# Kernel tuning notes

Measured on AMD Instinct MI355X. Metric: run time of the kernel, lower is better.

The kernel has to match this reference:

```python
import jax, jax.numpy as jnp
import numpy as np

T, B, H = 1024, 128, 256


def setup_inputs() -> dict:
    key = jax.random.key(0)
    k1, k2, k3, k4, k5 = jax.random.split(key, 5)
    ins = jax.random.normal(k1, (T, B, H), dtype=jnp.float32)
    resets = jax.random.randint(k2, (T, B), 0, 2).astype(jnp.bool_)
    # GRUCell params (flax layout): input dense (with bias) and recurrent dense
    # (bias only on the candidate 'hn' branch). Orthogonal-ish init approximated
    # by scaled normal for a pure-jnp reference.
    s = 1.0 / np.sqrt(H)
    Wi = jax.random.normal(k3, (H, 3 * H), dtype=jnp.float32) * s   # -> [ir|iz|in]
    Wh = jax.random.normal(k4, (H, 3 * H), dtype=jnp.float32) * s   # -> [hr|hz|hn]
    bi = jnp.zeros((3 * H,), dtype=jnp.float32)
    bhn = jnp.zeros((H,), dtype=jnp.float32)
    h0 = jnp.zeros((B, H), dtype=jnp.float32)  # initialize_carry -> zeros
    return {"ins": ins, "resets": resets, "h0": h0,
            "Wi": Wi, "Wh": Wh, "bi": bi, "bhn": bhn}


def reference(ins, resets, h0, Wi, Wh, bi, bhn):
    """ScannedRNN: GRU recurrence over time with per-step reset masking.

    ins: [T,B,H], resets: [T,B] bool, h0: [B,H]. Returns (final_carry, ys).
    """
    Hh = h0.shape[-1]

    def step(h, xt):
        x_t, r_t = xt                              # [B,H], [B]
        h = jnp.where(r_t[:, None], 0.0, h)        # reset carry to zeros
        gi = x_t @ Wi + bi                         # [B,3H]
        gh = h @ Wh                                # [B,3H]
        i_r, i_z, i_n = gi[:, :Hh], gi[:, Hh:2 * Hh], gi[:, 2 * Hh:]
        h_r, h_z, h_n = gh[:, :Hh], gh[:, Hh:2 * Hh], gh[:, 2 * Hh:]
        r = jax.nn.sigmoid(i_r + h_r)
        z = jax.nn.sigmoid(i_z + h_z)
        n = jnp.tanh(i_n + r * (h_n + bhn))
        h_new = (1.0 - z) * n + z * h
        return h_new, h_new                        # GRUCell returns (carry, y=carry)

    h_final, ys = jax.lax.scan(step, h0, (ins, resets))
    return h_final, ys
```

## Files before the change

### kernel.cpp

```cpp
#include <hip/hip_runtime.h>


typedef _Float16 half2_t __attribute__((ext_vector_type(2)));
typedef _Float16 half4_t __attribute__((ext_vector_type(4)));
typedef _Float16 half8_t __attribute__((ext_vector_type(8)));
typedef float f32x4 __attribute__((ext_vector_type(4)));

#define T_DIM 1024
#define B_DIM 128
#define H_DIM 256
#define N3 768
#define NSTREAM 4096
#define ROWS 16

__device__ __forceinline__ int perm_n(int cp) {
  int ublk = cp / 48;
  int rem = cp % 48;
  int g = rem >> 4;
  int u4 = rem & 15;
  return g * 256 + ublk * 16 + u4;
}


__global__ void prep_whb(const float* __restrict__ Wh, unsigned* __restrict__ WhB) {
  int i = blockIdx.x * 256 + threadIdx.x;
  int h = 2 * i;
  int idx = h & 7;
  int lane = (h >> 3) & 63;
  int ntk = h >> 9;
  int nt = ntk % 48;
  int kt = ntk / 48;
  int k = kt * 32 + ((lane >> 4) * 8) + idx;
  int n = perm_n(nt * 16 + (lane & 15));
  half2_t p;
  p.x = (_Float16)Wh[(size_t)k * N3 + n];
  p.y = (_Float16)Wh[(size_t)(k + 1) * N3 + n];
  WhB[i] = __builtin_bit_cast(unsigned, p);
}

__global__ void prep_witp(const float* __restrict__ Wi, _Float16* __restrict__ WiTp) {
  int i = blockIdx.x * 256 + threadIdx.x;
  int cp = i >> 8;
  int k = i & 255;
  WiTp[(size_t)cp * 256 + k] = (_Float16)Wi[(size_t)k * N3 + perm_n(cp)];
}

__global__ void prep_bip(const float* __restrict__ bi, float* __restrict__ bip) {
  int i = threadIdx.x;
  bip[i] = bi[perm_n(i)];
}

__global__ void init_h(const float* __restrict__ h0, float* __restrict__ h_state) {
  int i = blockIdx.x * 256 + threadIdx.x;
  h_state[i] = h0[i];
}

__global__ __launch_bounds__(256) void conv_a(
    const float* __restrict__ src, _Float16* __restrict__ dst, int n8) {
  int i = blockIdx.x * 256 + threadIdx.x;
  const int stride = gridDim.x * 256;
  for (; i < n8; i += stride) {
    float4 a = ((const float4*)src)[2 * i];
    float4 b = ((const float4*)src)[2 * i + 1];
    half8_t h;
    h[0] = (_Float16)a.x; h[1] = (_Float16)a.y;
    h[2] = (_Float16)a.z; h[3] = (_Float16)a.w;
    h[4] = (_Float16)b.x; h[5] = (_Float16)b.y;
    h[6] = (_Float16)b.z; h[7] = (_Float16)b.w;
    ((half8_t*)dst)[i] = h;
  }
}


__global__ void seg_transpose(const int* __restrict__ resets, int* __restrict__ resT) {
  int i = blockIdx.x * 256 + threadIdx.x;
  int b = i >> 10;
  int t = i & 1023;
  resT[i] = resets[(size_t)t * B_DIM + b];
}

__global__ __launch_bounds__(256) void seg_extract(
    const int* __restrict__ resT, int t0, int steps,
    unsigned* __restrict__ rowsegs, unsigned* __restrict__ rowcnt,
    unsigned* __restrict__ lhist) {
  const int b = blockIdx.x;
  const int tid = threadIdx.x;
  const int lane = tid & 63;
  const int w = tid >> 6;
  const int per = (steps + 255) >> 8;

  __shared__ unsigned short sstartL[1025];
  __shared__ unsigned lcur[1025];
  __shared__ unsigned wsum[4];

  for (int l = tid; l <= steps; l += 256) lcur[l] = 0;

  const int* rrow = resT + (size_t)b * T_DIM + t0;
  int myfirst = tid * per;
  unsigned cnt = 0;
  for (int i = 0; i < per; ++i) {
    int s = myfirst + i;
    if (s < steps && (s == 0 || rrow[s] != 0)) cnt++;
  }
  unsigned pre = cnt;
#pragma unroll
  for (int off = 1; off < 64; off <<= 1) {
    unsigned v = __shfl_up(pre, off);
    if (lane >= off) pre += v;
  }
  if (lane == 63) wsum[w] = pre;
  __syncthreads();
  unsigned wbase = 0, total = 0;
#pragma unroll
  for (int i = 0; i < 4; ++i) {
    if (i < w) wbase += wsum[i];
    total += wsum[i];
  }
  unsigned r = wbase + pre - cnt;
  for (int i = 0; i < per; ++i) {
    int s = myfirst + i;
    if (s < steps && (s == 0 || rrow[s] != 0)) sstartL[r++] = (unsigned short)s;
  }
  if (tid == 0) { sstartL[total] = (unsigned short)steps; rowcnt[b] = total; }
  __syncthreads();

  const unsigned carry0 = (rrow[0] == 0) ? 1u : 0u;
  for (unsigned rr = tid; rr < total; rr += 256) {
    int st = sstartL[rr];
    int len = (int)sstartL[rr + 1] - st;
    unsigned carry = (st == 0) ? carry0 : 0u;
    unsigned rk = atomicAdd(&lcur[len], 1u);
    rowsegs[(size_t)b * T_DIM + rr] =
        (unsigned)st | ((unsigned)len << 10) | (rk << 21) | (carry << 31);
  }
  __syncthreads();
  for (int l = tid; l <= steps; l += 256) lhist[(size_t)l * 128 + b] = lcur[l];
}

__global__ __launch_bounds__(1024) void seg_prefix2(
    const unsigned* __restrict__ lhist, unsigned* __restrict__ rowoff,
    unsigned* __restrict__ cursors, unsigned* __restrict__ Warr,
    unsigned* __restrict__ nseg, int steps) {
  __shared__ unsigned cs[1024];
  __shared__ unsigned cs2[1024];
  const int tid = threadIdx.x;
  const int len = tid + 1;
  unsigned run = 0;
  if (len <= steps) {
    for (int b = 0; b < 128; ++b) {
      rowoff[(size_t)len * 128 + b] = run;
      run += lhist[(size_t)len * 128 + b];
    }
  }
  unsigned own = run;
  unsigned own2 = run * (unsigned)len;
  cs[tid] = own;
  cs2[tid] = own2;
  for (int off = 1; off < 1024; off <<= 1) {
    __syncthreads();
    unsigned v = (tid + off < 1024) ? cs[tid + off] : 0u;
    unsigned v2 = (tid + off < 1024) ? cs2[tid + off] : 0u;
    __syncthreads();
    cs[tid] += v;
    cs2[tid] += v2;
  }
  cursors[len] = cs[tid] - own;
  Warr[len] = cs2[tid] - own2;
  if (tid == 0) *nseg = cs[0];
}

__global__ void seg_scatter2(
    const unsigned* __restrict__ rowsegs, const unsigned* __restrict__ rowcnt,
    const unsigned* __restrict__ rowoff, const unsigned* __restrict__ cursors,
    unsigned* __restrict__ segs) {
  int i = blockIdx.x * 256 + threadIdx.x;
  int b = i >> 10;
  int rr = i & 1023;
  if ((unsigned)rr >= rowcnt[b]) return;
  unsigned rec = rowsegs[i];
  unsigned st = rec & 0x3FF;
  unsigned len = (rec >> 10) & 0x7FF;
  unsigned rk = (rec >> 21) & 0x3FF;
  unsigned carry = rec >> 31;
  unsigned dst = cursors[len] + rowoff[(size_t)len * 128 + b] + rk;
  segs[dst] = st | (len << 10) | ((unsigned)b << 21) | (carry << 28);
}

__global__ void str_mark(
    const unsigned* __restrict__ segs, const unsigned* __restrict__ nseg_p,
    const unsigned* __restrict__ cursors, const unsigned* __restrict__ Warr,
    unsigned* __restrict__ sstart, unsigned* __restrict__ preexS, int Q) {
  unsigned r = blockIdx.x * 256 + threadIdx.x;
  unsigned n = *nseg_p;
  if (r >= n) return;
  unsigned rec = segs[r];
  unsigned len = (rec >> 10) & 0x7FF;
  unsigned pre = Warr[len] + len * (r - cursors[len]);
  unsigned st = pre / (unsigned)Q;
  unsigned stp;
  if (r == 0) {
    sstart[0] = 0; preexS[0] = 0; stp = 0;
  } else {
    unsigned rec2 = segs[r - 1];
    unsigned len2 = (rec2 >> 10) & 0x7FF;
    unsigned pre2 = Warr[len2] + len2 * (r - 1 - cursors[len2]);
    stp = pre2 / (unsigned)Q;
  }
  for (unsigned s = stp + 1; s <= st; ++s) { sstart[s] = r; preexS[s] = pre; }
}

__global__ __launch_bounds__(256) void gi_gemm(
    const _Float16* __restrict__ A16,
    const _Float16* __restrict__ BT,
    const float* __restrict__ bip,
    _Float16* __restrict__ Cout,
    int M) {
  __shared__ _Float16 Al[128 * 32];
  __shared__ _Float16 Bl[128 * 32];
  const int tid = threadIdx.x;
  const int lane = tid & 63;
  const int w = tid >> 6;
  const int wr = w >> 1, wc = w & 1;
  const int m0 = blockIdx.y * 128;
  const int n0 = blockIdx.x * 128;

  const int srow = lane >> 2;
  const int schunk = lane & 3;

  f32x4 acc[4][4] = {};

  for (int ks = 0; ks < 256; ks += 32) {
#pragma unroll
    for (int rr = 0; rr < 2; ++rr) {
      const int row = w * 32 + rr * 16;
      __builtin_amdgcn_global_load_lds(
          (const __attribute__((address_space(1))) void*)
              ((const char*)A16 + ((size_t)(m0 + row + srow) * 256 + ks) * 2 + schunk * 16),
          (__attribute__((address_space(3))) void*)((char*)Al + row * 64),
          16, 0, 0);
      __builtin_amdgcn_global_load_lds(
          (const __attribute__((address_space(1))) void*)
              ((const char*)BT + ((size_t)(n0 + row + srow) * 256 + ks) * 2 + schunk * 16),
          (__attribute__((address_space(3))) void*)((char*)Bl + row * 64),
          16, 0, 0);
    }
    __syncthreads();

    half8_t af[4], bf[4];
#pragma unroll
    for (int m = 0; m < 4; ++m)
      af[m] = *(const half8_t*)&Al[(size_t)(wr * 64 + m * 16 + (lane & 15)) * 32 + (lane >> 4) * 8];
#pragma unroll
    for (int n = 0; n < 4; ++n)
      bf[n] = *(const half8_t*)&Bl[(size_t)(wc * 64 + n * 16 + (lane & 15)) * 32 + (lane >> 4) * 8];
#pragma unroll
    for (int m = 0; m < 4; ++m)
#pragma unroll
      for (int n = 0; n < 4; ++n)
        acc[m][n] = __builtin_amdgcn_mfma_f32_16x16x32_f16(af[m], bf[n], acc[m][n], 0, 0, 0);
    __syncthreads();
  }

#pragma unroll
  for (int m = 0; m < 4; ++m) {
    int row = m0 + wr * 64 + m * 16 + (lane >> 4) * 4;
#pragma unroll
    for (int n = 0; n < 4; ++n) {
      int col = n0 + wc * 64 + n * 16 + (lane & 15);
      float bv = bip[col];
#pragma unroll
      for (int r2 = 0; r2 < 4; ++r2)
        Cout[(size_t)(row + r2) * N3 + col] = (_Float16)(acc[m][n][r2] + bv);
    }
  }
}

__global__ __launch_bounds__(512)
__attribute__((amdgpu_waves_per_eu(1, 2)))
void scan_stream(
    const _Float16* __restrict__ WhB,
    const _Float16* __restrict__ gi,
    const unsigned* __restrict__ segs,
    const unsigned* __restrict__ sstart,
    const unsigned* __restrict__ preexS,
    const unsigned* __restrict__ nseg_ptr,
    const float* __restrict__ bhn,
    const float* __restrict__ h_in,
    float* __restrict__ h_out,
    float* __restrict__ ys,
    float* __restrict__ hfin,
    int t0, int steps, int Q) {
  __shared__ _Float16 h_lds[ROWS][264];
  __shared__ _Float16 giL[ROWS][776];
  __shared__ unsigned rst[ROWS];
  __shared__ unsigned rowrank[ROWS];
  __shared__ unsigned rowpw[ROWS];
  __shared__ unsigned rfresh[ROWS];
  __shared__ unsigned wava[8];

  const int tid = threadIdx.x;
  const int lane = tid & 63;
  const int w = tid >> 6;
  const int sbase = blockIdx.x * ROWS;
  const unsigned nseg = *nseg_ptr;

  if (tid < ROWS) {
    const unsigned st = sbase + tid;
    unsigned r = sstart[st], pw = preexS[st];
    unsigned v = 0u, rk = 0xFFFFFFFFu, rpw = 0u;
    if (r < nseg && pw < (st + 1) * (unsigned)Q) {
      unsigned rec = segs[r];
      unsigned len = (rec >> 10) & 0x7FF;
      v = (rec & 0x3FF) | (((rec >> 21) & 0x7F) << 10) | (len << 17) |
          (((rec >> 28) & 1u) << 28);
      rk = r; rpw = pw + len;
    }
    rst[tid] = v; rowrank[tid] = rk; rowpw[tid] = rpw; rfresh[tid] = 0;
  }
  if (tid < 8) wava[tid] = 1u;

  half8_t whr[48];
#pragma unroll
  for (int kt = 0; kt < 8; ++kt)
#pragma unroll
    for (int q = 0; q < 6; ++q)
      whr[kt * 6 + q] =
          *(const half8_t*)&WhB[(((size_t)kt * 48 + w * 6 + q) * 64 + lane) * 8];

  __syncthreads();
#pragma unroll
  for (int rr = 0; rr < 2; ++rr) {
    int row = 2 * w + rr;
    unsigned s = rst[row];
    float4 o = make_float4(0.f, 0.f, 0.f, 0.f);
    if (s & (1u << 28))
      o = *(const float4*)&h_in[(size_t)((s >> 10) & 0x7F) * 256 + lane * 4];
    half4_t hv;
    hv.x = (_Float16)o.x; hv.y = (_Float16)o.y;
    hv.z = (_Float16)o.z; hv.w = (_Float16)o.w;
    *(half4_t*)&h_lds[row][lane * 4] = hv;
  }

  const int r16 = lane & 15;
  const int q4 = (lane >> 4) * 4;
  const int kq8 = (lane >> 4) * 8;
  const int u0 = w * 32 + r16;
  const float bh0 = bhn[u0];
  const float bh1 = bhn[u0 + 16];

  while (true) {
    __syncthreads();
    unsigned alive = 0;
#pragma unroll
    for (int i = 0; i < 8; ++i) alive += wava[i];
    if (!alive) break;

#pragma unroll
    for (int rr = 0; rr < 2; ++rr) {
      const int row = 2 * w + rr;
      const unsigned ss = rst[row];
      if ((ss >> 17) & 0x7FF) {
        const char* src = (const char*)(gi +
            ((size_t)(ss & 0x3FF) * B_DIM + ((ss >> 10) & 0x7F)) * N3);
        char* dst = (char*)&giL[row][0];
#if __has_builtin(__builtin_amdgcn_global_load_lds)
        __builtin_amdgcn_global_load_lds(
            (const __attribute__((address_space(1))) void*)(src + (size_t)lane * 16),
            (__attribute__((address_space(3))) void*)dst, 16, 0, 0);
        __builtin_amdgcn_global_load_lds(
            (const __attribute__((address_space(1))) void*)(src + 1024 + (size_t)lane * 4),
            (__attribute__((address_space(3))) void*)(dst + 1024), 4, 0, 0);
        __builtin_amdgcn_global_load_lds(
            (const __attribute__((address_space(1))) void*)(src + 1280 + (size_t)lane * 4),
            (__attribute__((address_space(3))) void*)(dst + 1280), 4, 0, 0);
#else
        {
          uint4 a = *(const uint4*)(src + ((size_t)(lane & 31)) * 48);
          uint4 b = *(const uint4*)(src + ((size_t)(lane & 31)) * 48 + 16);
          uint4 c = *(const uint4*)(src + ((size_t)(lane & 31)) * 48 + 32);
          if ((lane >> 5) == 0) {
            char* d2 = dst + ((size_t)(lane & 31)) * 48;
            *(uint4*)(d2) = a; *(uint4*)(d2 + 16) = b; *(uint4*)(d2 + 32) = c;
          }
        }
#endif
      }
    }

    f32x4 acc[6] = {};
#pragma unroll
    for (int kt = 0; kt < 8; ++kt) {
      half8_t afr = *(const half8_t*)&h_lds[r16][kt * 32 + kq8];
#pragma unroll
      for (int q = 0; q < 6; ++q)
        acc[q] = __builtin_amdgcn_mfma_f32_16x16x32_f16(afr, whr[kt * 6 + q], acc[q], 0, 0, 0);
    }
    __syncthreads();

#pragma unroll
    for (int j = 0; j < 2; ++j) {
      const int u = u0 + j * 16;
      const int cb = w * 96 + j * 48 + r16;
      const float bh = j ? bh1 : bh0;
#pragma unroll
      for (int e = 0; e < 4; ++e) {
        const int row = q4 + e;
        if ((rst[row] >> 17) & 0x7FF) {
          const float gr = (float)giL[row][cb];
          const float gz = (float)giL[row][cb + 16];
          const float gn = (float)giL[row][cb + 32];
          const float sigr = 1.f / (1.f + __expf(-(gr + acc[3 * j][e])));
          const float sigz = 1.f / (1.f + __expf(-(gz + acc[3 * j + 1][e])));
          const float narg = gn + sigr * (acc[3 * j + 2][e] + bh);
          const float eo = __expf(-2.f * narg);
          const float nn = 2.f / (1.f + eo) - 1.f;
          const float hold = (float)h_lds[row][u];
          const float hnew = (1.f - sigz) * nn + sigz * hold;
          h_lds[row][u] = (_Float16)hnew;
        }
      }
    }
    __syncthreads();

    unsigned alv = 0;
#pragma unroll
    for (int rr = 0; rr < 2; ++rr) {
      const int row = 2 * w + rr;
      const unsigned sp = rst[row];
      const unsigned rem = (sp >> 17) & 0x7FF;
      if (rem) {
        const int t = sp & 0x3FF;
        const int b = (sp >> 10) & 0x7F;
        half4_t hv = *(const half4_t*)&h_lds[row][lane * 4];
        float4 o;
        o.x = (float)hv.x; o.y = (float)hv.y; o.z = (float)hv.z; o.w = (float)hv.w;
        *(float4*)&ys[(((size_t)(t0 + t) * B_DIM + b) * H_DIM) + lane * 4] = o;
        if (rem == 1) {
          if (t == steps - 1) *(float4*)&h_out[(size_t)b * 256 + lane * 4] = o;
          if (t0 + t == T_DIM - 1) *(float4*)&hfin[(size_t)b * 256 + lane * 4] = o;
        }
        if (lane == 0) {
          rfresh[row] = 0u;
          if (rem > 1) {
            rst[row] = (unsigned)(t + 1) | ((unsigned)b << 10) | ((rem - 1) << 17);
            alv++;
          } else {
            unsigned ns = 0u;
            const unsigned st = sbase + row;
            unsigned rn = rowrank[row] + 1, pw = rowpw[row];
            if (rn < nseg && pw < (st + 1) * (unsigned)Q) {
              unsigned rec = segs[rn];
              unsigned len = (rec >> 10) & 0x7FF;
              ns = (rec & 0x3FF) | (((rec >> 21) & 0x7F) << 10) | (len << 17) |
                   (((rec >> 28) & 1u) << 28);
              rowrank[row] = rn; rowpw[row] = pw + len;
              rfresh[row] = 1u;
              alv++;
            }
            rst[row] = ns;
          }
        }
      }
    }
    if (lane == 0) wava[w] = alv;
#pragma unroll
    for (int rr = 0; rr < 2; ++rr) {
      const int row = 2 * w + rr;
      if (rfresh[row]) {
        unsigned s = rst[row];
        float4 o = make_float4(0.f, 0.f, 0.f, 0.f);
        if (s & (1u << 28))
          o = *(const float4*)&h_in[(size_t)((s >> 10) & 0x7F) * 256 + lane * 4];
        half4_t hv;
        hv.x = (_Float16)o.x; hv.y = (_Float16)o.y;
        hv.z = (_Float16)o.z; hv.w = (_Float16)o.w;
        *(half4_t*)&h_lds[row][lane * 4] = hv;
      }
    }
  }
}

extern "C" void kernel_launch(void* const* d_in, const int* in_sizes, int n_in,
                              void* d_out, int out_size, void* d_ws, size_t ws_size,
                              hipStream_t stream) {
  const float* ins    = (const float*)d_in[0];
  const int*   resets = (const int*)d_in[1];
  const float* h0     = (const float*)d_in[2];
  const float* Wi     = (const float*)d_in[3];
  const float* Wh     = (const float*)d_in[4];
  const float* bi     = (const float*)d_in[5];
  const float* bhn    = (const float*)d_in[6];
  float* out  = (float*)d_out;
  float* hfin = out;
  float* ys   = out + B_DIM * H_DIM;

  char* ws = (char*)d_ws;
  unsigned*  WhB     = (unsigned*)(ws + 0);
  _Float16*  WiTp    = (_Float16*)(ws + 393216);
  float*     bip     = (float*)(ws + 786432);
  float*     hA      = (float*)(ws + 789504);
  float*     hB      = (float*)(ws + 920576);
  int*       resT    = (int*)(ws + 1051648);
  unsigned*  rowsegs = (unsigned*)(ws + 1575936);
  unsigned*  rowcnt  = (unsigned*)(ws + 2100224);
  unsigned*  lhist   = (unsigned*)(ws + 2100736);
  unsigned*  rowoff  = (unsigned*)(ws + 2625536);
  unsigned*  cursors = (unsigned*)(ws + 3150336);
  unsigned*  Warr    = (unsigned*)(ws + 3154560);
  unsigned*  nseg    = (unsigned*)(ws + 3158784);
  unsigned*  segs    = (unsigned*)(ws + 3158912);
  unsigned*  sstart  = (unsigned*)(ws + 3683200);
  unsigned*  preexS  = (unsigned*)(ws + 3748736);
  const size_t gi_off = 3814400;

  int CH = T_DIM;
  while (CH > 256) {
    size_t need = gi_off + (size_t)CH * 128 * (N3 + H_DIM) * 2;
    if (need <= ws_size) break;
    CH >>= 1;
  }
  _Float16* gibuf = (_Float16*)(ws + gi_off);
  _Float16* A16   = (_Float16*)(ws + gi_off + (size_t)CH * 128 * N3 * 2);

  prep_whb<<<384, 256, 0, stream>>>(Wh, WhB);
  prep_witp<<<768, 256, 0, stream>>>(Wi, WiTp);
  prep_bip<<<1, 768, 0, stream>>>(bi, bip);
  init_h<<<128, 256, 0, stream>>>(h0, hA);
  seg_transpose<<<512, 256, 0, stream>>>(resets, resT);

  float* hbufs[2] = {hA, hB};
  for (int c = 0, t0 = 0; t0 < T_DIM; ++c, t0 += CH) {
    int steps = (t0 + CH <= T_DIM) ? CH : (T_DIM - t0);
    int M = steps * B_DIM;
    int Q = (M + NSTREAM - 1) / NSTREAM;
    if (Q < 1) Q = 1;

    conv_a<<<2048, 256, 0, stream>>>(ins + (size_t)t0 * B_DIM * H_DIM, A16, M * 32);

    dim3 ggrid(N3 / 128, M / 128);
    gi_gemm<<<ggrid, 256, 0, stream>>>(A16, WiTp, bip, gibuf, M);

    seg_extract<<<128, 256, 0, stream>>>(resT, t0, steps, rowsegs, rowcnt, lhist);
    seg_prefix2<<<1, 1024, 0, stream>>>(lhist, rowoff, cursors, Warr, nseg, steps);
    seg_scatter2<<<512, 256, 0, stream>>>(rowsegs, rowcnt, rowoff, cursors, segs);
    hipMemsetAsync(sstart, 0xFF, 131072, stream);
    str_mark<<<512, 256, 0, stream>>>(segs, nseg, cursors, Warr, sstart, preexS, Q);

    scan_stream<<<NSTREAM / ROWS, 512, 0, stream>>>(
        (const _Float16*)WhB, gibuf, segs, sstart, preexS, nseg, bhn,
        hbufs[c & 1], hbufs[(c + 1) & 1], ys, hfin, t0, steps, Q);
  }
}
```

Measured before the change: 417.1 us.

## Double-buffer gi prefetch and keep per-row segment state in registers

The gi staging buffer in LDS becomes double-buffered, and the next step's gate inputs are prefetched into the alternate buffer while the current step's MFMA and gate math run. Per-row segment state (current/next record, rank, position, next segment record) moves from shared memory into per-wave registers, and the next segments record is prefetched one ahead. __syncthreads calls are replaced by explicit waitcnt plus s_barrier, so the global-to-LDS loads can stay in flight across the mid-step barriers. This roughly doubles the gi LDS footprint and makes correctness depend on hand-placed waitcnts.

Result: no change. 422.8 us (+1.4%).

```diff
diff --git a/kernel.cpp b/kernel.cpp
--- a/kernel.cpp
+++ b/kernel.cpp
@@ -291,11 +291,10 @@
     float* __restrict__ hfin,
     int t0, int steps, int Q) {
   __shared__ _Float16 h_lds[ROWS][264];
-  __shared__ _Float16 giL[ROWS][776];
+  __shared__ _Float16 giL[2][ROWS][776];
   __shared__ unsigned rst[ROWS];
-  __shared__ unsigned rowrank[ROWS];
-  __shared__ unsigned rowpw[ROWS];
-  __shared__ unsigned rfresh[ROWS];
+  __shared__ unsigned rowrankL[ROWS];
+  __shared__ unsigned rowpwL[ROWS];
   __shared__ unsigned wava[8];
 
   const int tid = threadIdx.x;
@@ -307,15 +306,15 @@
   if (tid < ROWS) {
     const unsigned st = sbase + tid;
     unsigned r = sstart[st], pw = preexS[st];
-    unsigned v = 0u, rk = 0xFFFFFFFFu, rpw = 0u;
+    unsigned v = 0u, rk = 0xFFFFFFFFu, rpw0 = 0u;
     if (r < nseg && pw < (st + 1) * (unsigned)Q) {
       unsigned rec = segs[r];
       unsigned len = (rec >> 10) & 0x7FF;
       v = (rec & 0x3FF) | (((rec >> 21) & 0x7F) << 10) | (len << 17) |
           (((rec >> 28) & 1u) << 28);
-      rk = r; rpw = pw + len;
-    }
-    rst[tid] = v; rowrank[tid] = rk; rowpw[tid] = rpw; rfresh[tid] = 0;
+      rk = r; rpw0 = pw + len;
+    }
+    rst[tid] = v; rowrankL[tid] = rk; rowpwL[tid] = rpw0;
   }
   if (tid < 8) wava[tid] = 1u;
 
@@ -328,10 +327,25 @@
           *(const half8_t*)&WhB[(((size_t)kt * 48 + w * 6 + q) * 64 + lane) * 8];
 
   __syncthreads();
+
+  unsigned rcur[2], rnxt[2], rrk[2], rpw[2], segnx[2], lim[2];
+  unsigned rfr[2];
+#pragma unroll
+  for (int rr = 0; rr < 2; ++rr) {
+    const int row = 2 * w + rr;
+    rcur[rr] = rst[row];
+    rrk[rr]  = rowrankL[row];
+    rpw[rr]  = rowpwL[row];
+    lim[rr]  = (unsigned)(sbase + row + 1) * (unsigned)Q;
+    unsigned rn2 = rrk[rr] + 1;
+    unsigned i2 = (rn2 < nseg) ? rn2 : (nseg - 1);
+    segnx[rr] = segs[i2];
+  }
+
 #pragma unroll
   for (int rr = 0; rr < 2; ++rr) {
     int row = 2 * w + rr;
-    unsigned s = rst[row];
+    unsigned s = rcur[rr];
     float4 o = make_float4(0.f, 0.f, 0.f, 0.f);
     if (s & (1u << 28))
       o = *(const float4*)&h_in[(size_t)((s >> 10) & 0x7F) * 256 + lane * 4];
@@ -341,6 +355,38 @@
     *(half4_t*)&h_lds[row][lane * 4] = hv;
   }
 
+#pragma unroll
+  for (int rr = 0; rr < 2; ++rr) {
+    const int row = 2 * w + rr;
+    const unsigned ss = rcur[rr];
+    if ((ss >> 17) & 0x7FF) {
+      const char* src = (const char*)(gi +
+          ((size_t)(ss & 0x3FF) * B_DIM + ((ss >> 10) & 0x7F)) * N3);
+      char* dst = (char*)&giL[0][row][0];
+#if __has_builtin(__builtin_amdgcn_global_load_lds)
+      __builtin_amdgcn_global_load_lds(
+          (const __attribute__((address_space(1))) void*)(src + (size_t)lane * 16),
+          (__attribute__((address_space(3))) void*)dst, 16, 0, 0);
+      __builtin_amdgcn_global_load_lds(
+          (const __attribute__((address_space(1))) void*)(src + 1024 + (size_t)lane * 4),
+          (__attribute__((address_space(3))) void*)(dst + 1024), 4, 0, 0);
+      __builtin_amdgcn_global_load_lds(
+          (const __attribute__((address_space(1))) void*)(src + 1280 + (size_t)lane * 4),
+          (__attribute__((address_space(3))) void*)(dst + 1280), 4, 0, 0);
+#else
+      {
+        uint4 a = *(const uint4*)(src + ((size_t)(lane & 31)) * 48);
+        uint4 b = *(const uint4*)(src + ((size_t)(lane & 31)) * 48 + 16);
+        uint4 c = *(const uint4*)(src + ((size_t)(lane & 31)) * 48 + 32);
+        if ((lane >> 5) == 0) {
+          char* d2 = dst + ((size_t)(lane & 31)) * 48;
+          *(uint4*)(d2) = a; *(uint4*)(d2 + 16) = b; *(uint4*)(d2 + 32) = c;
+        }
+      }
+#endif
+    }
+  }
+
   const int r16 = lane & 15;
   const int q4 = (lane >> 4) * 4;
   const int kq8 = (lane >> 4) * 8;
@@ -348,8 +394,13 @@
   const float bh0 = bhn[u0];
   const float bh1 = bhn[u0 + 16];
 
+  int cur = 0;
   while (true) {
-    __syncthreads();
+    asm volatile("s_waitcnt vmcnt(0)" ::: "memory");
+    asm volatile("s_waitcnt lgkmcnt(0)" ::: "memory");
+    __builtin_amdgcn_s_barrier();
+    __builtin_amdgcn_sched_barrier(0);
+
     unsigned alive = 0;
 #pragma unroll
     for (int i = 0; i < 8; ++i) alive += wava[i];
@@ -357,12 +408,38 @@
 
 #pragma unroll
     for (int rr = 0; rr < 2; ++rr) {
+      const unsigned cs = rcur[rr];
+      const unsigned rem = (cs >> 17) & 0x7FF;
+      unsigned nx = 0u;
+      rfr[rr] = 0u;
+      if (rem > 1) {
+        nx = ((cs & 0x3FF) + 1) | (cs & (0x7Fu << 10)) | ((rem - 1) << 17);
+      } else if (rem == 1) {
+        unsigned rn = rrk[rr] + 1;
+        unsigned pw = rpw[rr];
+        if (rn < nseg && pw < lim[rr]) {
+          unsigned rec = segnx[rr];
+          unsigned len = (rec >> 10) & 0x7FF;
+          nx = (rec & 0x3FF) | (((rec >> 21) & 0x7F) << 10) | (len << 17) |
+               (((rec >> 28) & 1u) << 28);
+          rrk[rr] = rn; rpw[rr] = pw + len;
+          rfr[rr] = 1u;
+          unsigned rn2 = rn + 1;
+          unsigned i2 = (rn2 < nseg) ? rn2 : (nseg - 1);
+          segnx[rr] = segs[i2];
+        }
+      }
+      rnxt[rr] = nx;
+    }
+
+#pragma unroll
+    for (int rr = 0; rr < 2; ++rr) {
       const int row = 2 * w + rr;
-      const unsigned ss = rst[row];
+      const unsigned ss = rnxt[rr];
       if ((ss >> 17) & 0x7FF) {
         const char* src = (const char*)(gi +
             ((size_t)(ss & 0x3FF) * B_DIM + ((ss >> 10) & 0x7F)) * N3);
-        char* dst = (char*)&giL[row][0];
+        char* dst = (char*)&giL[cur ^ 1][row][0];
 #if __has_builtin(__builtin_amdgcn_global_load_lds)
         __builtin_amdgcn_global_load_lds(
             (const __attribute__((address_space(1))) void*)(src + (size_t)lane * 16),
@@ -395,7 +472,10 @@
       for (int q = 0; q < 6; ++q)
         acc[q] = __builtin_amdgcn_mfma_f32_16x16x32_f16(afr, whr[kt * 6 + q], acc[q], 0, 0, 0);
     }
-    __syncthreads();
+
+    asm volatile("s_waitcnt lgkmcnt(0)" ::: "memory");
+    __builtin_amdgcn_s_barrier();
+    __builtin_amdgcn_sched_barrier(0);
 
 #pragma unroll
     for (int j = 0; j < 2; ++j) {
@@ -406,9 +486,9 @@
       for (int e = 0; e < 4; ++e) {
         const int row = q4 + e;
         if ((rst[row] >> 17) & 0x7FF) {
-          const float gr = (float)giL[row][cb];
-          const float gz = (float)giL[row][cb + 16];
-          const float gn = (float)giL[row][cb + 32];
+          const float gr = (float)giL[cur][row][cb];
+          const float gz = (float)giL[cur][row][cb + 16];
+          const float gn = (float)giL[cur][row][cb + 32];
           const float sigr = 1.f / (1.f + __expf(-(gr + acc[3 * j][e])));
           const float sigz = 1.f / (1.f + __expf(-(gz + acc[3 * j + 1][e])));
           const float narg = gn + sigr * (acc[3 * j + 2][e] + bh);
@@ -420,13 +500,16 @@
         }
       }
     }
-    __syncthreads();
+
+    asm volatile("s_waitcnt lgkmcnt(0)" ::: "memory");
+    __builtin_amdgcn_s_barrier();
+    __builtin_amdgcn_sched_barrier(0);
 
     unsigned alv = 0;
 #pragma unroll
     for (int rr = 0; rr < 2; ++rr) {
       const int row = 2 * w + rr;
-      const unsigned sp = rst[row];
+      const unsigned sp = rcur[rr];
       const unsigned rem = (sp >> 17) & 0x7FF;
       if (rem) {
         const int t = sp & 0x3FF;
@@ -439,44 +522,24 @@
           if (t == steps - 1) *(float4*)&h_out[(size_t)b * 256 + lane * 4] = o;
           if (t0 + t == T_DIM - 1) *(float4*)&hfin[(size_t)b * 256 + lane * 4] = o;
         }
-        if (lane == 0) {
-          rfresh[row] = 0u;
-          if (rem > 1) {
-            rst[row] = (unsigned)(t + 1) | ((unsigned)b << 10) | ((rem - 1) << 17);
-            alv++;
-          } else {
-            unsigned ns = 0u;
-            const unsigned st = sbase + row;
-            unsigned rn = rowrank[row] + 1, pw = rowpw[row];
-            if (rn < nseg && pw < (st + 1) * (unsigned)Q) {
-              unsigned rec = segs[rn];
-              unsigned len = (rec >> 10) & 0x7FF;
-              ns = (rec & 0x3FF) | (((rec >> 21) & 0x7F) << 10) | (len << 17) |
-                   (((rec >> 28) & 1u) << 28);
-              rowrank[row] = rn; rowpw[row] = pw + len;
-              rfresh[row] = 1u;
-              alv++;
-            }
-            rst[row] = ns;
-          }
-        }
       }
+      if ((rnxt[rr] >> 17) & 0x7FF) alv++;
+      rcur[rr] = rnxt[rr];
+      if (lane == 0) rst[row] = rnxt[rr];
+      if (rfr[rr]) {
+        unsigned s = rnxt[rr];
+        float4 o2 = make_float4(0.f, 0.f, 0.f, 0.f);
+        if (s & (1u << 28))
+          o2 = *(const float4*)&h_in[(size_t)((s >> 10) & 0x7F) * 256 + lane * 4];
+        half4_t hv2;
+        hv2.x = (_Float16)o2.x; hv2.y = (_Float16)o2.y;
+        hv2.z = (_Float16)o2.z; hv2.w = (_Float16)o2.w;
+        *(half4_t*)&h_lds[row][lane * 4] = hv2;
+      }
     }
     if (lane == 0) wava[w] = alv;
-#pragma unroll
-    for (int rr = 0; rr < 2; ++rr) {
-      const int row = 2 * w + rr;
-      if (rfresh[row]) {
-        unsigned s = rst[row];
-        float4 o = make_float4(0.f, 0.f, 0.f, 0.f);
-        if (s & (1u << 28))
-          o = *(const float4*)&h_in[(size_t)((s >> 10) & 0x7F) * 256 + lane * 4];
-        half4_t hv;
-        hv.x = (_Float16)o.x; hv.y = (_Float16)o.y;
-        hv.z = (_Float16)o.z; hv.w = (_Float16)o.w;
-        *(half4_t*)&h_lds[row][lane * 4] = hv;
-      }
-    }
+
+    cur ^= 1;
   }
 }
 
```
